# Performance work log

Hardware: AMD Instinct MI355X
Metric: run time of the kernel (lower is better)

The kernel has to match this reference:

```python
import jax, jax.numpy as jnp
import numpy as np

EPS = 1e-5  # BatchNorm2d default eps; running stats at init: mean=0, var=1


def conv_bn_silu(x, w, gamma, beta):
    # 1x1 conv (no bias) + BatchNorm (mean=0, var=1) + SiLU
    y = jnp.einsum('bchw,oc->bohw', x, w)
    y = y * (gamma / jnp.sqrt(1.0 + EPS))[None, :, None, None] + beta[None, :, None, None]
    return jax.nn.silu(y)


def setup_inputs() -> dict:
    key = jax.random.key(0)
    ks = jax.random.split(key, 13)
    c1, c2 = 256, 256
    ci = c2 // 8   # 32  (theta/phi)
    cg = c2 // 2   # 128 (g)
    b, h, w = 8, 56, 56
    sd = lambda cin: 1.0 / np.sqrt(cin)
    return {
        'x':       jax.random.normal(ks[0], (b, c1, h, w), jnp.float32),
        'w_theta': jax.random.normal(ks[1], (ci, c1), jnp.float32) * sd(c1),
        'g_theta': jnp.ones((ci,), jnp.float32),
        'b_theta': jnp.zeros((ci,), jnp.float32),
        'w_phi':   jax.random.normal(ks[2], (ci, c1), jnp.float32) * sd(c1),
        'g_phi':   jnp.ones((ci,), jnp.float32),
        'b_phi':   jnp.zeros((ci,), jnp.float32),
        'w_g':     jax.random.normal(ks[3], (cg, c1), jnp.float32) * sd(c1),
        'g_g':     jnp.ones((cg,), jnp.float32),
        'b_g':     jnp.zeros((cg,), jnp.float32),
        'w_out':   jax.random.normal(ks[4], (c2, cg), jnp.float32) * sd(cg),
        'g_out':   jnp.ones((c2,), jnp.float32),
        'b_out':   jnp.zeros((c2,), jnp.float32),
    }


def reference(x, w_theta, g_theta, b_theta, w_phi, g_phi, b_phi,
              w_g, g_g, b_g, w_out, g_out, b_out):
    b, c, h, w = x.shape
    hw = h * w
    theta = conv_bn_silu(x, w_theta, g_theta, b_theta).reshape(b, -1, hw).transpose(0, 2, 1)  # [b,hw,ci]
    phi   = conv_bn_silu(x, w_phi,   g_phi,   b_phi).reshape(b, -1, hw)                       # [b,ci,hw]
    g     = conv_bn_silu(x, w_g,     g_g,     b_g).reshape(b, -1, hw).transpose(0, 2, 1)      # [b,hw,cg]
    attn = jax.nn.softmax(jnp.einsum('bnc,bcm->bnm', theta, phi), axis=-1)                    # [b,hw,hw]
    out = jnp.einsum('bnm,bmc->bnc', attn, g).transpose(0, 2, 1).reshape(b, -1, h, w)         # [b,cg,h,w]
    return conv_bn_silu(out, w_out, g_out, b_out) + x
```

## Files before the change

### kernel.cpp

```cpp
#include <hip/hip_runtime.h>

typedef __bf16 bf16;
typedef __bf16 bf16x4 __attribute__((ext_vector_type(4)));
typedef __bf16 bf16x8 __attribute__((ext_vector_type(8)));
typedef float f32x4 __attribute__((ext_vector_type(4)));

#define MFMA16(a,b,c) __builtin_amdgcn_mfma_f32_16x16x32_bf16((a),(b),(c),0,0,0)
#define NSPLIT 7

__device__ __forceinline__ float silu_f(float y){ return y/(1.f+__expf(-y)); }

template<int CTRL>
__device__ __forceinline__ float ror_max(float x){
    int y = __builtin_amdgcn_update_dpp(0, __builtin_bit_cast(int,x), CTRL, 0xf, 0xf, false);
    return fmaxf(x, __builtin_bit_cast(float,y));
}
template<int CTRL>
__device__ __forceinline__ float ror_add(float x){
    int y = __builtin_amdgcn_update_dpp(0, __builtin_bit_cast(int,x), CTRL, 0xf, 0xf, false);
    return x + __builtin_bit_cast(float,y);
}
__device__ __forceinline__ float red16_max(float x){
    x = ror_max<0x128>(x); x = ror_max<0x124>(x);
    x = ror_max<0x122>(x); x = ror_max<0x121>(x); return x;
}
__device__ __forceinline__ float red16_add(float x){
    x = ror_add<0x128>(x); x = ror_add<0x124>(x);
    x = ror_add<0x122>(x); x = ror_add<0x121>(x); return x;
}

__device__ __forceinline__ bf16x8 ld8f(const float* __restrict__ p){
    float4 a = *(const float4*)p;
    float4 b = *(const float4*)(p+4);
    bf16x8 r;
    r[0]=(bf16)a.x; r[1]=(bf16)a.y; r[2]=(bf16)a.z; r[3]=(bf16)a.w;
    r[4]=(bf16)b.x; r[5]=(bf16)b.y; r[6]=(bf16)b.z; r[7]=(bf16)b.w;
    return r;
}

#define BN_SCALE 0.9999950000374997f

__global__ __launch_bounds__(256) void qkv_kernel(
    const float* __restrict__ xg,
    const float* __restrict__ wth, const float* __restrict__ gth, const float* __restrict__ bth,
    const float* __restrict__ wph, const float* __restrict__ gph, const float* __restrict__ bph,
    const float* __restrict__ wgg, const float* __restrict__ ggg, const float* __restrict__ bgg,
    bf16* __restrict__ Qb, bf16* __restrict__ Kb, bf16* __restrict__ Vtb)
{
    const int b = blockIdx.x, pt = blockIdx.y;
    const int p0 = pt*32;
    const int t = threadIdx.x;
    const int lane = t & 63, wv = t >> 6;
    const int lc = lane & 15, lg = lane >> 4;

    __shared__ __align__(16) bf16 xT[32][264];

    {
        const int ci = t & 15;
        const int pj = (t >> 4) & 7;
        const int ch = t >> 7;
        const int p4 = pj*4;
        #pragma unroll
        for (int r = 0; r < 2; ++r) {
            const int c0 = (r*2 + ch)*64 + ci*4;
            float va[4][4];
            #pragma unroll
            for (int k = 0; k < 4; ++k) {
                float4 v = *(const float4*)(xg + ((size_t)(b*256 + c0 + k))*3136 + p0 + p4);
                va[k][0]=v.x; va[k][1]=v.y; va[k][2]=v.z; va[k][3]=v.w;
            }
            #pragma unroll
            for (int i = 0; i < 4; ++i) {
                bf16x4 w;
                w[0]=(bf16)va[0][i]; w[1]=(bf16)va[1][i];
                w[2]=(bf16)va[2][i]; w[3]=(bf16)va[3][i];
                *(bf16x4*)&xT[p4+i][c0] = w;
            }
        }
    }
    __syncthreads();

    const f32x4 fz = {0.f,0.f,0.f,0.f};

    for (int tt = 0; tt < 3; ++tt) {
        const int ot = wv*3 + tt;
        if (ot < 4) {
            const float *W, *gam, *bet; bf16* dst; int ol;
            if (ot < 2) { W=wth; gam=gth; bet=bth; dst=Qb; ol=ot*16; }
            else        { W=wph; gam=gph; bet=bph; dst=Kb; ol=(ot-2)*16; }
            f32x4 acc[2]; acc[0]=fz; acc[1]=fz;
            #pragma unroll
            for (int ks = 0; ks < 8; ++ks) {
                bf16x8 wf = ld8f(W + (size_t)(ol+lc)*256 + ks*32 + lg*8);
                #pragma unroll
                for (int pf = 0; pf < 2; ++pf) {
                    bf16x8 af = *(const bf16x8*)&xT[pf*16+lc][ks*32+lg*8];
                    acc[pf] = MFMA16(af, wf, acc[pf]);
                }
            }
            const int oc = ol + lc;
            const float sc = gam[oc] * BN_SCALE;
            const float bi = bet[oc];
            #pragma unroll
            for (int pf = 0; pf < 2; ++pf)
                #pragma unroll
                for (int r = 0; r < 4; ++r) {
                    int pos = p0 + pf*16 + lg*4 + r;
                    dst[((size_t)b*3136 + pos)*32 + oc] = (bf16)silu_f(acc[pf][r]*sc + bi);
                }
        } else {
            const int ol = (ot-4)*16;
            f32x4 acc[2]; acc[0]=fz; acc[1]=fz;
            #pragma unroll
            for (int ks = 0; ks < 8; ++ks) {
                bf16x8 wf = ld8f(wgg + (size_t)(ol+lc)*256 + ks*32 + lg*8);
                #pragma unroll
                for (int pc = 0; pc < 2; ++pc) {
                    bf16x8 xf = *(const bf16x8*)&xT[pc*16+lc][ks*32+lg*8];
                    acc[pc] = MFMA16(wf, xf, acc[pc]);
                }
            }
            #pragma unroll
            for (int r = 0; r < 4; ++r) {
                const int oc = ol + lg*4 + r;
                const float sc = ggg[oc] * BN_SCALE;
                const float bi = bgg[oc];
                #pragma unroll
                for (int pc = 0; pc < 2; ++pc) {
                    int pos = p0 + pc*16 + lc;
                    Vtb[((size_t)b*128 + oc)*3136 + pos] = (bf16)silu_f(acc[pc][r]*sc + bi);
                }
            }
        }
    }
}

__global__ __launch_bounds__(256) void attn_kernel(
    const bf16* __restrict__ Qb, const bf16* __restrict__ Kb,
    const bf16* __restrict__ Vtb, bf16* __restrict__ Opart,
    float* __restrict__ mpart, float* __restrict__ lpart)
{
    const int b = blockIdx.x, qt = blockIdx.y, z = blockIdx.z;
    const int kt0 = z*7, kt1 = kt0+7;
    const int p0 = qt*64;
    const int t = threadIdx.x;
    const int lane = t & 63, wv = t >> 6;
    const int lc = lane & 15, lg = lane >> 4;

    __shared__ __align__(16) bf16 Klds[2][64][40];
    __shared__ __align__(16) bf16 Vlds[2][128*64];
    __shared__ __align__(16) bf16 Plds[4][16*72];

    const bf16* Kbase = Kb + (size_t)b*3136*32;
    const bf16* Vbase = Vtb + (size_t)b*128*3136;

    bf16x8 qf = *(const bf16x8*)(Qb + ((size_t)b*3136 + p0 + wv*16 + lc)*32 + lg*8);

    float mrow[4] = {-1e30f,-1e30f,-1e30f,-1e30f};
    float lrow[4] = {0.f,0.f,0.f,0.f};
    const f32x4 fz = {0.f,0.f,0.f,0.f};
    f32x4 oacc[8];
    #pragma unroll
    for (int cf = 0; cf < 8; ++cf) oacc[cf] = fz;

    const int krow = t >> 2, kkp = (t & 3) * 8;
    const int vrow0 = t >> 3, vj = t & 7;
    const int vxor = (vrow0 & 7) << 4;
    const int pxorw = (lg >> 1) << 4;
    const int pxorr = (lc >> 3) << 4;

    bf16x8 kreg, vreg0, vreg1, vreg2, vreg3;
    {
        const int k0 = kt0*64;
        kreg  = *(const bf16x8*)(Kbase + (size_t)(k0+krow)*32 + kkp);
        vreg0 = *(const bf16x8*)(Vbase + (size_t)(0*32+vrow0)*3136 + k0 + vj*8);
        vreg1 = *(const bf16x8*)(Vbase + (size_t)(1*32+vrow0)*3136 + k0 + vj*8);
        vreg2 = *(const bf16x8*)(Vbase + (size_t)(2*32+vrow0)*3136 + k0 + vj*8);
        vreg3 = *(const bf16x8*)(Vbase + (size_t)(3*32+vrow0)*3136 + k0 + vj*8);
    }

    int cur = 0;
    for (int kt = kt0; kt < kt1; ++kt) {
        bf16* Kl = &Klds[cur][0][0];
        bf16* Vl = &Vlds[cur][0];
        *(bf16x8*)&Kl[krow*40 + kkp] = kreg;
        *(bf16x8*)((char*)Vl + (0*32+vrow0)*128 + ((vj*16) ^ vxor)) = vreg0;
        *(bf16x8*)((char*)Vl + (1*32+vrow0)*128 + ((vj*16) ^ vxor)) = vreg1;
        *(bf16x8*)((char*)Vl + (2*32+vrow0)*128 + ((vj*16) ^ vxor)) = vreg2;
        *(bf16x8*)((char*)Vl + (3*32+vrow0)*128 + ((vj*16) ^ vxor)) = vreg3;
        __syncthreads();

        if (kt+1 < kt1) {
            const int kn = (kt+1)*64;
            kreg  = *(const bf16x8*)(Kbase + (size_t)(kn+krow)*32 + kkp);
            vreg0 = *(const bf16x8*)(Vbase + (size_t)(0*32+vrow0)*3136 + kn + vj*8);
            vreg1 = *(const bf16x8*)(Vbase + (size_t)(1*32+vrow0)*3136 + kn + vj*8);
            vreg2 = *(const bf16x8*)(Vbase + (size_t)(2*32+vrow0)*3136 + kn + vj*8);
            vreg3 = *(const bf16x8*)(Vbase + (size_t)(3*32+vrow0)*3136 + kn + vj*8);
        }

        f32x4 s[4];
        #pragma unroll
        for (int nf = 0; nf < 4; ++nf) {
            bf16x8 kf = *(const bf16x8*)&Kl[(nf*16+lc)*40 + lg*8];
            s[nf] = MFMA16(qf, kf, fz);
        }

        float mx[4];
        #pragma unroll
        for (int r = 0; r < 4; ++r) {
            float m = fmaxf(fmaxf(s[0][r], s[1][r]), fmaxf(s[2][r], s[3][r]));
            mx[r] = red16_max(m);
        }
        bool ok = (mx[0] <= mrow[0]+8.f) && (mx[1] <= mrow[1]+8.f)
               && (mx[2] <= mrow[2]+8.f) && (mx[3] <= mrow[3]+8.f);
        if (!__all(ok)) {
            float scale[4];
            #pragma unroll
            for (int r = 0; r < 4; ++r) {
                float nm = fmaxf(mrow[r], mx[r]);
                scale[r] = __expf(mrow[r] - nm);
                mrow[r] = nm;
                lrow[r] *= scale[r];
            }
            #pragma unroll
            for (int cf = 0; cf < 8; ++cf)
                #pragma unroll
                for (int r = 0; r < 4; ++r) oacc[cf][r] *= scale[r];
        }
        #pragma unroll
        for (int r = 0; r < 4; ++r) {
            float ps = 0.f;
            #pragma unroll
            for (int nf = 0; nf < 4; ++nf) {
                float pv = __expf(s[nf][r] - mrow[r]); s[nf][r] = pv; ps += pv;
            }
            lrow[r] += red16_add(ps);
        }

        #pragma unroll
        for (int nf = 0; nf < 4; ++nf)
            #pragma unroll
            for (int r = 0; r < 4; ++r)
                Plds[wv][(lg*4+r)*72 + ((nf*16+lc) ^ pxorw)] = (bf16)s[nf][r];

        __builtin_amdgcn_s_setprio(1);
        #pragma unroll
        for (int ks = 0; ks < 2; ++ks) {
            bf16x8 pfr = *(const bf16x8*)&Plds[wv][lc*72 + ((ks*32 + lg*8) ^ pxorr)];
            #pragma unroll
            for (int cf = 0; cf < 8; ++cf) {
                const int vrow = cf*16 + lc;
                bf16x8 vf = *(const bf16x8*)((char*)Vl + vrow*128
                                 + ((ks*64 + lg*16) ^ ((vrow & 7) << 4)));
                oacc[cf] = MFMA16(pfr, vf, oacc[cf]);
            }
        }
        __builtin_amdgcn_s_setprio(0);
        cur ^= 1;
    }

    #pragma unroll
    for (int cf = 0; cf < 8; ++cf)
        #pragma unroll
        for (int r = 0; r < 4; ++r) {
            int q = p0 + wv*16 + lg*4 + r;
            Opart[((size_t)(z*8+b)*3136 + q)*128 + cf*16 + lc] = (bf16)oacc[cf][r];
        }
    if (lc == 0) {
        #pragma unroll
        for (int r = 0; r < 4; ++r) {
            int q = p0 + wv*16 + lg*4 + r;
            size_t idx = (size_t)(z*8+b)*3136 + q;
            mpart[idx] = mrow[r];
            lpart[idx] = lrow[r];
        }
    }
}

__global__ __launch_bounds__(256) void out_kernel(
    const bf16* __restrict__ Opart, const float* __restrict__ mpart,
    const float* __restrict__ lpart, const float* __restrict__ wout,
    const float* __restrict__ gout, const float* __restrict__ bout,
    const float* __restrict__ xg, float* __restrict__ outp)
{
    const int b = blockIdx.x, pt = blockIdx.y;
    const int p0 = pt*32;
    const int t = threadIdx.x;
    const int lane = t & 63, wv = t >> 6;
    const int lc = lane & 15, lg = lane >> 4;

    __shared__ __align__(16) bf16 Olds[32][136];
    __shared__ __align__(16) bf16 outlds[4][64][40];

    {
        const int row = t >> 3;
        const int cc  = (t & 7) * 16;
        const int q = p0 + row;
        float mz[NSPLIT], wz[NSPLIT];
        float M = -1e30f;
        #pragma unroll
        for (int zz = 0; zz < NSPLIT; ++zz) {
            mz[zz] = mpart[(size_t)(zz*8+b)*3136 + q];
            M = fmaxf(M, mz[zz]);
        }
        float L = 0.f;
        #pragma unroll
        for (int zz = 0; zz < NSPLIT; ++zz) {
            wz[zz] = __expf(mz[zz] - M);
            L += lpart[(size_t)(zz*8+b)*3136 + q] * wz[zz];
        }
        const float inv = 1.f / L;
        #pragma unroll
        for (int zz = 0; zz < NSPLIT; ++zz) wz[zz] *= inv;
        #pragma unroll
        for (int h = 0; h < 2; ++h) {
            const int c8 = cc + h*8;
            float o[8];
            #pragma unroll
            for (int j = 0; j < 8; ++j) o[j] = 0.f;
            #pragma unroll
            for (int zz = 0; zz < NSPLIT; ++zz) {
                bf16x8 v = *(const bf16x8*)(Opart + ((size_t)(zz*8+b)*3136 + q)*128 + c8);
                #pragma unroll
                for (int j = 0; j < 8; ++j) o[j] += wz[zz] * (float)v[j];
            }
            bf16x8 rr;
            #pragma unroll
            for (int j = 0; j < 8; ++j) rr[j] = (bf16)o[j];
            *(bf16x8*)&Olds[row][c8] = rr;
        }
    }
    __syncthreads();

    const f32x4 fz = {0.f,0.f,0.f,0.f};
    f32x4 acc[2][4];
    #pragma unroll
    for (int pf = 0; pf < 2; ++pf)
        #pragma unroll
        for (int nf = 0; nf < 4; ++nf) acc[pf][nf] = fz;

    #pragma unroll
    for (int ks = 0; ks < 4; ++ks) {
        bf16x8 wf[4];
        #pragma unroll
        for (int nf = 0; nf < 4; ++nf)
            wf[nf] = ld8f(wout + (size_t)(wv*64 + nf*16 + lc)*128 + ks*32 + lg*8);
        #pragma unroll
        for (int pf = 0; pf < 2; ++pf) {
            bf16x8 af = *(const bf16x8*)&Olds[pf*16+lc][ks*32+lg*8];
            #pragma unroll
            for (int nf = 0; nf < 4; ++nf)
                acc[pf][nf] = MFMA16(af, wf[nf], acc[pf][nf]);
        }
    }

    #pragma unroll
    for (int nf = 0; nf < 4; ++nf) {
        const int oc = wv*64 + nf*16 + lc;
        const float sc = gout[oc] * BN_SCALE;
        const float bi = bout[oc];
        #pragma unroll
        for (int pf = 0; pf < 2; ++pf) {
            bf16x4 w;
            #pragma unroll
            for (int r = 0; r < 4; ++r)
                w[r] = (bf16)silu_f(acc[pf][nf][r]*sc + bi);
            *(bf16x4*)&outlds[wv][nf*16+lc][pf*16+lg*4] = w;
        }
    }

    #pragma unroll
    for (int i = 0; i < 8; ++i) {
        const int orow = i*8 + (lane >> 3);
        const int oc = wv*64 + orow;
        const int p4 = (lane & 7) * 4;
        bf16x4 vo = *(const bf16x4*)&outlds[wv][orow][p4];
        float4 vx = *(const float4*)(xg + ((size_t)b*256 + oc)*3136 + p0 + p4);
        float4 res;
        res.x = (float)vo[0] + vx.x;
        res.y = (float)vo[1] + vx.y;
        res.z = (float)vo[2] + vx.z;
        res.w = (float)vo[3] + vx.w;
        *(float4*)(outp + ((size_t)b*256 + oc)*3136 + p0 + p4) = res;
    }
}

extern "C" void kernel_launch(void* const* d_in, const int* in_sizes, int n_in,
                              void* d_out, int out_size, void* d_ws, size_t ws_size,
                              hipStream_t stream)
{
    const float* x    = (const float*)d_in[0];
    const float* wth  = (const float*)d_in[1];
    const float* gth  = (const float*)d_in[2];
    const float* bth  = (const float*)d_in[3];
    const float* wph  = (const float*)d_in[4];
    const float* gph  = (const float*)d_in[5];
    const float* bph  = (const float*)d_in[6];
    const float* wgg  = (const float*)d_in[7];
    const float* ggg  = (const float*)d_in[8];
    const float* bgg  = (const float*)d_in[9];
    const float* wout = (const float*)d_in[10];
    const float* gout = (const float*)d_in[11];
    const float* bout = (const float*)d_in[12];

    bf16* ws  = (bf16*)d_ws;
    bf16* Qb    = ws;
    bf16* Kb    = Qb + (size_t)8*3136*32;
    bf16* Vtb   = Kb + (size_t)8*3136*32;
    bf16* Opart = Vtb + (size_t)8*128*3136;
    float* mpart = (float*)(Opart + (size_t)NSPLIT*8*3136*128);
    float* lpart = mpart + (size_t)NSPLIT*8*3136;

    dim3 blk(256);
    qkv_kernel<<<dim3(8,98), blk, 0, stream>>>(x, wth, gth, bth, wph, gph, bph,
                                               wgg, ggg, bgg, Qb, Kb, Vtb);
    attn_kernel<<<dim3(8,49,NSPLIT), blk, 0, stream>>>(Qb, Kb, Vtb, Opart, mpart, lpart);
    out_kernel<<<dim3(8,98), blk, 0, stream>>>(Opart, mpart, lpart,
                                               wout, gout, bout, x, (float*)d_out);
}
```

Baseline: 214.8 us.

## Double pixel tile in qkv and out kernels, fold log2e into Q for exp2

The qkv and out kernels now process 64 pixels per block instead of 32, halving the grid and reusing each weight fragment load across twice as many MFMAs. Q is prescaled by log2(e) at projection time so the attention softmax and the split merge can use the native exp2 instruction instead of __expf, and the rescale threshold is adjusted to the base-2 domain. Larger tiles raise LDS and register use and leave fewer blocks per kernel. Q is now rounded to bf16 after the log2(e) scaling, which changes the rounding slightly.

```diff
diff --git a/kernel.cpp b/kernel.cpp
--- a/kernel.cpp
+++ b/kernel.cpp
@@ -7,8 +7,10 @@
 
 #define MFMA16(a,b,c) __builtin_amdgcn_mfma_f32_16x16x32_bf16((a),(b),(c),0,0,0)
 #define NSPLIT 7
+#define LOG2E 1.4426950408889634f
 
 __device__ __forceinline__ float silu_f(float y){ return y/(1.f+__expf(-y)); }
+__device__ __forceinline__ float exp2_f(float x){ return __builtin_amdgcn_exp2f(x); }
 
 template<int CTRL>
 __device__ __forceinline__ float ror_max(float x){
@@ -48,34 +50,32 @@
     bf16* __restrict__ Qb, bf16* __restrict__ Kb, bf16* __restrict__ Vtb)
 {
     const int b = blockIdx.x, pt = blockIdx.y;
-    const int p0 = pt*32;
+    const int p0 = pt*64;
     const int t = threadIdx.x;
     const int lane = t & 63, wv = t >> 6;
     const int lc = lane & 15, lg = lane >> 4;
 
-    __shared__ __align__(16) bf16 xT[32][264];
+    __shared__ __align__(16) bf16 xT[64][264];
 
     {
-        const int ci = t & 15;
-        const int pj = (t >> 4) & 7;
-        const int ch = t >> 7;
-        const int p4 = pj*4;
-        #pragma unroll
-        for (int r = 0; r < 2; ++r) {
-            const int c0 = (r*2 + ch)*64 + ci*4;
-            float va[4][4];
-            #pragma unroll
-            for (int k = 0; k < 4; ++k) {
-                float4 v = *(const float4*)(xg + ((size_t)(b*256 + c0 + k))*3136 + p0 + p4);
-                va[k][0]=v.x; va[k][1]=v.y; va[k][2]=v.z; va[k][3]=v.w;
-            }
-            #pragma unroll
-            for (int i = 0; i < 4; ++i) {
-                bf16x4 w;
-                w[0]=(bf16)va[0][i]; w[1]=(bf16)va[1][i];
-                w[2]=(bf16)va[2][i]; w[3]=(bf16)va[3][i];
-                *(bf16x4*)&xT[p4+i][c0] = w;
-            }
+        const int p4 = (t & 15) * 4;
+        const int cq = t >> 4;
+        #pragma unroll
+        for (int r = 0; r < 4; ++r) {
+            const int c0 = r*64 + cq*4;
+            float4 v0 = *(const float4*)(xg + ((size_t)(b*256 + c0+0))*3136 + p0 + p4);
+            float4 v1 = *(const float4*)(xg + ((size_t)(b*256 + c0+1))*3136 + p0 + p4);
+            float4 v2 = *(const float4*)(xg + ((size_t)(b*256 + c0+2))*3136 + p0 + p4);
+            float4 v3 = *(const float4*)(xg + ((size_t)(b*256 + c0+3))*3136 + p0 + p4);
+            bf16x4 w;
+            w[0]=(bf16)v0.x; w[1]=(bf16)v1.x; w[2]=(bf16)v2.x; w[3]=(bf16)v3.x;
+            *(bf16x4*)&xT[p4+0][c0] = w;
+            w[0]=(bf16)v0.y; w[1]=(bf16)v1.y; w[2]=(bf16)v2.y; w[3]=(bf16)v3.y;
+            *(bf16x4*)&xT[p4+1][c0] = w;
+            w[0]=(bf16)v0.z; w[1]=(bf16)v1.z; w[2]=(bf16)v2.z; w[3]=(bf16)v3.z;
+            *(bf16x4*)&xT[p4+2][c0] = w;
+            w[0]=(bf16)v0.w; w[1]=(bf16)v1.w; w[2]=(bf16)v2.w; w[3]=(bf16)v3.w;
+            *(bf16x4*)&xT[p4+3][c0] = w;
         }
     }
     __syncthreads();
@@ -85,15 +85,15 @@
     for (int tt = 0; tt < 3; ++tt) {
         const int ot = wv*3 + tt;
         if (ot < 4) {
-            const float *W, *gam, *bet; bf16* dst; int ol;
-            if (ot < 2) { W=wth; gam=gth; bet=bth; dst=Qb; ol=ot*16; }
-            else        { W=wph; gam=gph; bet=bph; dst=Kb; ol=(ot-2)*16; }
-            f32x4 acc[2]; acc[0]=fz; acc[1]=fz;
+            const float *W, *gam, *bet; bf16* dst; int ol; float post;
+            if (ot < 2) { W=wth; gam=gth; bet=bth; dst=Qb; ol=ot*16; post=LOG2E; }
+            else        { W=wph; gam=gph; bet=bph; dst=Kb; ol=(ot-2)*16; post=1.f; }
+            f32x4 acc[4]; acc[0]=fz; acc[1]=fz; acc[2]=fz; acc[3]=fz;
             #pragma unroll
             for (int ks = 0; ks < 8; ++ks) {
                 bf16x8 wf = ld8f(W + (size_t)(ol+lc)*256 + ks*32 + lg*8);
                 #pragma unroll
-                for (int pf = 0; pf < 2; ++pf) {
+                for (int pf = 0; pf < 4; ++pf) {
                     bf16x8 af = *(const bf16x8*)&xT[pf*16+lc][ks*32+lg*8];
                     acc[pf] = MFMA16(af, wf, acc[pf]);
                 }
@@ -102,20 +102,21 @@
             const float sc = gam[oc] * BN_SCALE;
             const float bi = bet[oc];
             #pragma unroll
-            for (int pf = 0; pf < 2; ++pf)
+            for (int pf = 0; pf < 4; ++pf)
                 #pragma unroll
                 for (int r = 0; r < 4; ++r) {
                     int pos = p0 + pf*16 + lg*4 + r;
-                    dst[((size_t)b*3136 + pos)*32 + oc] = (bf16)silu_f(acc[pf][r]*sc + bi);
+                    dst[((size_t)b*3136 + pos)*32 + oc] =
+                        (bf16)(silu_f(acc[pf][r]*sc + bi) * post);
                 }
         } else {
             const int ol = (ot-4)*16;
-            f32x4 acc[2]; acc[0]=fz; acc[1]=fz;
+            f32x4 acc[4]; acc[0]=fz; acc[1]=fz; acc[2]=fz; acc[3]=fz;
             #pragma unroll
             for (int ks = 0; ks < 8; ++ks) {
                 bf16x8 wf = ld8f(wgg + (size_t)(ol+lc)*256 + ks*32 + lg*8);
                 #pragma unroll
-                for (int pc = 0; pc < 2; ++pc) {
+                for (int pc = 0; pc < 4; ++pc) {
                     bf16x8 xf = *(const bf16x8*)&xT[pc*16+lc][ks*32+lg*8];
                     acc[pc] = MFMA16(wf, xf, acc[pc]);
                 }
@@ -126,7 +127,7 @@
                 const float sc = ggg[oc] * BN_SCALE;
                 const float bi = bgg[oc];
                 #pragma unroll
-                for (int pc = 0; pc < 2; ++pc) {
+                for (int pc = 0; pc < 4; ++pc) {
                     int pos = p0 + pc*16 + lc;
                     Vtb[((size_t)b*128 + oc)*3136 + pos] = (bf16)silu_f(acc[pc][r]*sc + bi);
                 }
@@ -212,14 +213,14 @@
             float m = fmaxf(fmaxf(s[0][r], s[1][r]), fmaxf(s[2][r], s[3][r]));
             mx[r] = red16_max(m);
         }
-        bool ok = (mx[0] <= mrow[0]+8.f) && (mx[1] <= mrow[1]+8.f)
-               && (mx[2] <= mrow[2]+8.f) && (mx[3] <= mrow[3]+8.f);
+        bool ok = (mx[0] <= mrow[0]+11.5416f) && (mx[1] <= mrow[1]+11.5416f)
+               && (mx[2] <= mrow[2]+11.5416f) && (mx[3] <= mrow[3]+11.5416f);
         if (!__all(ok)) {
             float scale[4];
             #pragma unroll
             for (int r = 0; r < 4; ++r) {
                 float nm = fmaxf(mrow[r], mx[r]);
-                scale[r] = __expf(mrow[r] - nm);
+                scale[r] = exp2_f(mrow[r] - nm);
                 mrow[r] = nm;
                 lrow[r] *= scale[r];
             }
@@ -233,7 +234,7 @@
             float ps = 0.f;
             #pragma unroll
             for (int nf = 0; nf < 4; ++nf) {
-                float pv = __expf(s[nf][r] - mrow[r]); s[nf][r] = pv; ps += pv;
+                float pv = exp2_f(s[nf][r] - mrow[r]); s[nf][r] = pv; ps += pv;
             }
             lrow[r] += red16_add(ps);
         }
@@ -285,17 +286,17 @@
     const float* __restrict__ xg, float* __restrict__ outp)
 {
     const int b = blockIdx.x, pt = blockIdx.y;
-    const int p0 = pt*32;
+    const int p0 = pt*64;
     const int t = threadIdx.x;
     const int lane = t & 63, wv = t >> 6;
     const int lc = lane & 15, lg = lane >> 4;
 
-    __shared__ __align__(16) bf16 Olds[32][136];
-    __shared__ __align__(16) bf16 outlds[4][64][40];
+    __shared__ __align__(16) bf16 Olds[64][136];
+    __shared__ __align__(16) bf16 outlds[4][64][72];
 
     {
-        const int row = t >> 3;
-        const int cc  = (t & 7) * 16;
+        const int row = t >> 2;
+        const int cb = (t & 3) * 32;
         const int q = p0 + row;
         float mz[NSPLIT], wz[NSPLIT];
         float M = -1e30f;
@@ -307,15 +308,15 @@
         float L = 0.f;
         #pragma unroll
         for (int zz = 0; zz < NSPLIT; ++zz) {
-            wz[zz] = __expf(mz[zz] - M);
+            wz[zz] = exp2_f(mz[zz] - M);
             L += lpart[(size_t)(zz*8+b)*3136 + q] * wz[zz];
         }
         const float inv = 1.f / L;
         #pragma unroll
         for (int zz = 0; zz < NSPLIT; ++zz) wz[zz] *= inv;
         #pragma unroll
-        for (int h = 0; h < 2; ++h) {
-            const int c8 = cc + h*8;
+        for (int h = 0; h < 4; ++h) {
+            const int c8 = cb + h*8;
             float o[8];
             #pragma unroll
             for (int j = 0; j < 8; ++j) o[j] = 0.f;
@@ -334,9 +335,9 @@
     __syncthreads();
 
     const f32x4 fz = {0.f,0.f,0.f,0.f};
-    f32x4 acc[2][4];
-    #pragma unroll
-    for (int pf = 0; pf < 2; ++pf)
+    f32x4 acc[4][4];
+    #pragma unroll
+    for (int pf = 0; pf < 4; ++pf)
         #pragma unroll
         for (int nf = 0; nf < 4; ++nf) acc[pf][nf] = fz;
 
@@ -347,7 +348,7 @@
         for (int nf = 0; nf < 4; ++nf)
             wf[nf] = ld8f(wout + (size_t)(wv*64 + nf*16 + lc)*128 + ks*32 + lg*8);
         #pragma unroll
-        for (int pf = 0; pf < 2; ++pf) {
+        for (int pf = 0; pf < 4; ++pf) {
             bf16x8 af = *(const bf16x8*)&Olds[pf*16+lc][ks*32+lg*8];
             #pragma unroll
             for (int nf = 0; nf < 4; ++nf)
@@ -361,7 +362,7 @@
         const float sc = gout[oc] * BN_SCALE;
         const float bi = bout[oc];
         #pragma unroll
-        for (int pf = 0; pf < 2; ++pf) {
+        for (int pf = 0; pf < 4; ++pf) {
             bf16x4 w;
             #pragma unroll
             for (int r = 0; r < 4; ++r)
@@ -371,10 +372,10 @@
     }
 
     #pragma unroll
-    for (int i = 0; i < 8; ++i) {
-        const int orow = i*8 + (lane >> 3);
+    for (int i = 0; i < 16; ++i) {
+        const int orow = i*4 + lg;
         const int oc = wv*64 + orow;
-        const int p4 = (lane & 7) * 4;
+        const int p4 = lc*4;
         bf16x4 vo = *(const bf16x4*)&outlds[wv][orow][p4];
         float4 vx = *(const float4*)(xg + ((size_t)b*256 + oc)*3136 + p0 + p4);
         float4 res;
@@ -413,9 +414,9 @@
     float* lpart = mpart + (size_t)NSPLIT*8*3136;
 
     dim3 blk(256);
-    qkv_kernel<<<dim3(8,98), blk, 0, stream>>>(x, wth, gth, bth, wph, gph, bph,
+    qkv_kernel<<<dim3(8,49), blk, 0, stream>>>(x, wth, gth, bth, wph, gph, bph,
                                                wgg, ggg, bgg, Qb, Kb, Vtb);
     attn_kernel<<<dim3(8,49,NSPLIT), blk, 0, stream>>>(Qb, Kb, Vtb, Opart, mpart, lpart);
-    out_kernel<<<dim3(8,98), blk, 0, stream>>>(Opart, mpart, lpart,
+    out_kernel<<<dim3(8,49), blk, 0, stream>>>(Opart, mpart, lpart,
                                                wout, gout, bout, x, (float*)d_out);
 }
```

After: 197.4 us. -8.1%, faster.
